# Optimization experiments

Measured on AMD Instinct MI355X. Metric: run time of the kernel, lower is better.

The kernel has to match this reference:

```python
import jax, jax.numpy as jnp
import numpy as np

N_NODES = 500000


def _gconv(x, src, dst, ew, w_neigh, b, w_self):
    # DGL GraphConv(norm='none'): multiply weight first (in>=out here), then aggregate.
    h = x @ w_neigh                      # [N, out]
    msg = h[src] * ew[:, None]           # [E, out]
    agg = jax.ops.segment_sum(msg, dst, num_segments=N_NODES)
    return agg + b + x @ w_self          # neigh conv (+bias) + self-loop linear (no bias)


def setup_inputs() -> dict:
    key = jax.random.key(0)
    ks = jax.random.split(key, 16)
    N, E, G, F = N_NODES, 16000000, 64, 16
    inp = {
        "x": jax.random.normal(ks[0], (N, F), jnp.float32),
        "src": jax.random.randint(ks[1], (E,), 0, N),
        "dst": jax.random.randint(ks[2], (E,), 0, N),
        "graph_id": jnp.sort(jax.random.randint(ks[3], (N,), 0, G)),
        "edge_weight": jax.random.uniform(ks[4], (E,), jnp.float32),
        "num_graphs": G,
        "w_neigh0": jax.random.normal(ks[5], (F, 1), jnp.float32),
        "b0": jax.random.normal(ks[6], (1,), jnp.float32),
        "w_self0": jax.random.normal(ks[7], (F, 1), jnp.float32),
        "w_neigh1": jax.random.normal(ks[8], (1, 1), jnp.float32),
        "b1": jax.random.normal(ks[9], (1,), jnp.float32),
        "w_self1": jax.random.normal(ks[10], (1, 1), jnp.float32),
        "w_neigh2": jax.random.normal(ks[11], (1, 1), jnp.float32),
        "b2": jax.random.normal(ks[12], (1,), jnp.float32),
        "w_self2": jax.random.normal(ks[13], (1, 1), jnp.float32),
        "fc1_w": jax.random.normal(ks[14], (8, 1), jnp.float32),
        "fc1_b": jax.random.normal(ks[15], (8,), jnp.float32),
        "out_w": jax.random.normal(jax.random.fold_in(key, 100), (4, 8), jnp.float32),
        "out_b": jax.random.normal(jax.random.fold_in(key, 101), (4,), jnp.float32),
    }
    return inp


def reference(x, src, dst, graph_id, edge_weight, num_graphs,
              w_neigh0, b0, w_self0, w_neigh1, b1, w_self1,
              w_neigh2, b2, w_self2, fc1_w, fc1_b, out_w, out_b):
    h = jax.nn.relu(_gconv(x, src, dst, edge_weight, w_neigh0, b0, w_self0))
    h = jax.nn.relu(_gconv(h, src, dst, edge_weight, w_neigh1, b1, w_self1))
    h = jax.nn.relu(_gconv(h, src, dst, edge_weight, w_neigh2, b2, w_self2))
    # dgl.sum_nodes: per-graph segment sum over batched graph -> [G, 1]
    hg = jax.ops.segment_sum(h, graph_id, num_segments=num_graphs)
    hg2 = jax.nn.sigmoid((hg @ fc1_w.T + fc1_b) * 1000.0)   # [G, 8]
    out = jax.nn.relu(hg2 @ out_w.T + out_b)                # [G, 4]
    return jax.nn.log_softmax(out, axis=1)
```

## Files before the change

### kernel.cpp

```cpp
#include <hip/hip_runtime.h>

#define N_NODES   500000
#define NGRAPH    64
#define FDIM      16
#define NPB       4096
#define NPB_SHIFT 12
#define NBINS     123
#define SLICES    4
#define NBLK      256
typedef unsigned int u32;
typedef unsigned long long u64;

__global__ void proj_kernel(const float* __restrict__ x,
                            const float* __restrict__ wn,
                            const float* __restrict__ wsf,
                            float* __restrict__ a,
                            float* __restrict__ s) {
    int i = blockIdx.x * blockDim.x + threadIdx.x;
    if (i >= N_NODES) return;
    const float4* xr = (const float4*)(x + (size_t)i * FDIM);
    float4 v0 = xr[0], v1 = xr[1], v2 = xr[2], v3 = xr[3];
    const float4* n4 = (const float4*)wn;
    const float4* s4 = (const float4*)wsf;
    float4 n0 = n4[0], n1 = n4[1], n2 = n4[2], n3 = n4[3];
    float4 w0 = s4[0], w1 = s4[1], w2 = s4[2], w3 = s4[3];
    float an = v0.x*n0.x + v0.y*n0.y + v0.z*n0.z + v0.w*n0.w
             + v1.x*n1.x + v1.y*n1.y + v1.z*n1.z + v1.w*n1.w
             + v2.x*n2.x + v2.y*n2.y + v2.z*n2.z + v2.w*n2.w
             + v3.x*n3.x + v3.y*n3.y + v3.z*n3.z + v3.w*n3.w;
    float as = v0.x*w0.x + v0.y*w0.y + v0.z*w0.z + v0.w*w0.w
             + v1.x*w1.x + v1.y*w1.y + v1.z*w1.z + v1.w*w1.w
             + v2.x*w2.x + v2.y*w2.y + v2.z*w2.z + v2.w*w2.w
             + v3.x*w3.x + v3.y*w3.y + v3.z*w3.z + v3.w*w3.w;
    a[i] = an;
    s[i] = as;
}

__global__ __launch_bounds__(1024) void hist_kernel(const int* __restrict__ dst, int E, int chunk,
                                                    u32* __restrict__ blockHist) {
    __shared__ u32 cnt[NBINS];
    for (int t = threadIdx.x; t < NBINS; t += 1024) cnt[t] = 0;
    __syncthreads();
    int b = blockIdx.x;
    int lo = b * chunk, hi = min(lo + chunk, E);
    int m = (hi - lo) & ~3;
    for (int i = lo + threadIdx.x * 4; i < lo + m; i += 4096) {
        int4 d = *(const int4*)(dst + i);
        atomicAdd(&cnt[((u32)d.x) >> NPB_SHIFT], 1u);
        atomicAdd(&cnt[((u32)d.y) >> NPB_SHIFT], 1u);
        atomicAdd(&cnt[((u32)d.z) >> NPB_SHIFT], 1u);
        atomicAdd(&cnt[((u32)d.w) >> NPB_SHIFT], 1u);
    }
    for (int i = lo + m + threadIdx.x; i < hi; i += 1024)
        atomicAdd(&cnt[((u32)dst[i]) >> NPB_SHIFT], 1u);
    __syncthreads();
    for (int t = threadIdx.x; t < NBINS; t += 1024)
        blockHist[(size_t)b * NBINS + t] = cnt[t];
}

__global__ __launch_bounds__(NBLK) void scan1_kernel(u32* __restrict__ blockHist,
                                                     u32* __restrict__ binTotal) {
    int j = blockIdx.x;
    __shared__ u32 lsum[NBLK];
    int t = threadIdx.x;
    u32 v = blockHist[(size_t)t * NBINS + j];
    lsum[t] = v;
    __syncthreads();
    u32 x = v;
    for (int off = 1; off < NBLK; off <<= 1) {
        u32 y = (t >= off) ? lsum[t - off] : 0u;
        __syncthreads();
        x += y; lsum[t] = x;
        __syncthreads();
    }
    if (t == NBLK - 1) binTotal[j] = x;
    blockHist[(size_t)t * NBINS + j] = x - v;
}

__global__ void scan2_kernel(const u32* __restrict__ binTotal, u32* __restrict__ binStart) {
    if (threadIdx.x == 0) {
        u32 run = 0;
        for (int j = 0; j < NBINS; ++j) { binStart[j] = run; run += binTotal[j]; }
        binStart[NBINS] = run;
    }
}

__global__ __launch_bounds__(1024) void scatter_kernel(const int* __restrict__ src,
                                                       const int* __restrict__ dst,
                                                       const float* __restrict__ ew,
                                                       int E, int chunk,
                                                       const u32* __restrict__ blockHist,
                                                       const u32* __restrict__ binStart,
                                                       u64* __restrict__ binned) {
    __shared__ u32 pos[NBINS];
    int b = blockIdx.x;
    for (int t = threadIdx.x; t < NBINS; t += 1024)
        pos[t] = binStart[t] + blockHist[(size_t)b * NBINS + t];
    __syncthreads();
    int lo = b * chunk, hi = min(lo + chunk, E);
    int m = (hi - lo) & ~3;
    for (int i = lo + threadIdx.x * 4; i < lo + m; i += 4096) {
        int4   ss = *(const int4*)(src + i);
        int4   dd = *(const int4*)(dst + i);
        float4 ww = *(const float4*)(ew + i);
        u32 d0 = (u32)dd.x, d1 = (u32)dd.y, d2 = (u32)dd.z, d3 = (u32)dd.w;
        u32 p0 = atomicAdd(&pos[d0 >> NPB_SHIFT], 1u);
        u32 p1 = atomicAdd(&pos[d1 >> NPB_SHIFT], 1u);
        u32 p2 = atomicAdd(&pos[d2 >> NPB_SHIFT], 1u);
        u32 p3 = atomicAdd(&pos[d3 >> NPB_SHIFT], 1u);
        u32 r0 = ((u32)ss.x) | ((d0 & (NPB-1)) << 19);
        u32 r1 = ((u32)ss.y) | ((d1 & (NPB-1)) << 19);
        u32 r2 = ((u32)ss.z) | ((d2 & (NPB-1)) << 19);
        u32 r3 = ((u32)ss.w) | ((d3 & (NPB-1)) << 19);
        binned[p0] = (u64)r0 | ((u64)__float_as_uint(ww.x) << 32);
        binned[p1] = (u64)r1 | ((u64)__float_as_uint(ww.y) << 32);
        binned[p2] = (u64)r2 | ((u64)__float_as_uint(ww.z) << 32);
        binned[p3] = (u64)r3 | ((u64)__float_as_uint(ww.w) << 32);
    }
    for (int i = lo + m + threadIdx.x; i < hi; i += 1024) {
        u32 d = (u32)dst[i];
        u32 p = atomicAdd(&pos[d >> NPB_SHIFT], 1u);
        binned[p] = (u64)(((u32)src[i]) | ((d & (NPB-1)) << 19))
                  | ((u64)__float_as_uint(ew[i]) << 32);
    }
}

__global__ __launch_bounds__(512) void bin_pass(const u64* __restrict__ binned,
                                                const u32* __restrict__ binStart,
                                                const float* __restrict__ hsrc,
                                                float* __restrict__ partials) {
    __shared__ float acc[NPB];
    int blk   = blockIdx.x;
    int j     = blk >> 2;
    int slice = blk & (SLICES - 1);
    for (int t = threadIdx.x; t < NPB; t += 512) acc[t] = 0.0f;
    __syncthreads();
    u32 blo = binStart[j], bhi = binStart[j + 1];
    u32 cnt = bhi - blo;
    u32 per = (cnt + SLICES - 1) / SLICES;
    u32 lo = blo + slice * per;
    u32 hi = min(lo + per, bhi);

    u32 i = lo + threadIdx.x;
    for (; i + 3u * 512u < hi; i += 4u * 512u) {
        u64 e0 = __builtin_nontemporal_load(&binned[i]);
        u64 e1 = __builtin_nontemporal_load(&binned[i + 512]);
        u64 e2 = __builtin_nontemporal_load(&binned[i + 1024]);
        u64 e3 = __builtin_nontemporal_load(&binned[i + 1536]);
        u32 x0 = (u32)e0, x1 = (u32)e1, x2 = (u32)e2, x3 = (u32)e3;
        float g0 = hsrc[x0 & 0x7FFFFu];
        float g1 = hsrc[x1 & 0x7FFFFu];
        float g2 = hsrc[x2 & 0x7FFFFu];
        float g3 = hsrc[x3 & 0x7FFFFu];
        atomicAdd(&acc[x0 >> 19], g0 * __uint_as_float((u32)(e0 >> 32)));
        atomicAdd(&acc[x1 >> 19], g1 * __uint_as_float((u32)(e1 >> 32)));
        atomicAdd(&acc[x2 >> 19], g2 * __uint_as_float((u32)(e2 >> 32)));
        atomicAdd(&acc[x3 >> 19], g3 * __uint_as_float((u32)(e3 >> 32)));
    }
    for (; i < hi; i += 512) {
        u64 e = __builtin_nontemporal_load(&binned[i]);
        u32 xx = (u32)e;
        atomicAdd(&acc[xx >> 19], hsrc[xx & 0x7FFFFu] * __uint_as_float((u32)(e >> 32)));
    }
    __syncthreads();
    float* p = partials + (size_t)(j * SLICES + slice) * NPB;
    for (int t = threadIdx.x; t < NPB; t += 512)
        __builtin_nontemporal_store(acc[t], &p[t]);
}

__global__ void merge_update(const float* __restrict__ partials,
                             const float* __restrict__ selfv,
                             const float* __restrict__ wnp,
                             const float* __restrict__ bp,
                             const float* __restrict__ wsp,
                             float* __restrict__ hout) {
    int n = blockIdx.x * blockDim.x + threadIdx.x;
    if (n >= N_NODES) return;
    int j = n >> NPB_SHIFT;
    int l = n & (NPB - 1);
    const float* p = partials + (size_t)j * SLICES * NPB + l;
    float sum = p[0] + p[NPB] + p[2 * NPB] + p[3 * NPB];
    float scale = wnp ? wnp[0] : 1.0f;
    float wself = wsp ? wsp[0] : 1.0f;
    hout[n] = fmaxf(sum * scale + bp[0] + selfv[n] * wself, 0.0f);
}

__global__ void edge_pass(const int* __restrict__ src, const int* __restrict__ dst,
                          const float* __restrict__ ew, const float* __restrict__ h,
                          float* __restrict__ agg, const float* __restrict__ wnp, int E) {
    float scale = wnp ? wnp[0] : 1.0f;
    int stride = gridDim.x * blockDim.x;
    for (int i = blockIdx.x * blockDim.x + threadIdx.x; i < E; i += stride)
        atomicAdd(&agg[dst[i]], h[src[i]] * ew[i] * scale);
}
__global__ void node_update(const float* __restrict__ agg, const float* __restrict__ selfv,
                            const float* __restrict__ bp, const float* __restrict__ wsp,
                            float* __restrict__ hout) {
    int i = blockIdx.x * blockDim.x + threadIdx.x;
    if (i >= N_NODES) return;
    float wsc = wsp ? wsp[0] : 1.0f;
    hout[i] = fmaxf(agg[i] + bp[0] + selfv[i] * wsc, 0.0f);
}

__global__ void graph_sum(const float* __restrict__ h, const int* __restrict__ gid,
                          float* __restrict__ hg) {
    __shared__ float loc[NGRAPH];
    int t = threadIdx.x;
    if (t < NGRAPH) loc[t] = 0.0f;
    __syncthreads();
    int stride = gridDim.x * blockDim.x;
    for (int i = blockIdx.x * blockDim.x + t; i < N_NODES; i += stride)
        atomicAdd(&loc[gid[i]], h[i]);
    __syncthreads();
    if (t < NGRAPH) atomicAdd(&hg[t], loc[t]);
}

__global__ void head_kernel(const float* __restrict__ hg,
                            const float* __restrict__ fc1w, const float* __restrict__ fc1b,
                            const float* __restrict__ outw, const float* __restrict__ outb,
                            float* __restrict__ out) {
    int g = threadIdx.x;
    if (g >= NGRAPH) return;
    float v = hg[g];
    float t[8];
#pragma unroll
    for (int j = 0; j < 8; ++j) {
        float z = (v * fc1w[j] + fc1b[j]) * 1000.0f;
        t[j] = 1.0f / (1.0f + expf(-z));
    }
    float o[4];
#pragma unroll
    for (int k = 0; k < 4; ++k) {
        float acc2 = outb[k];
#pragma unroll
        for (int j = 0; j < 8; ++j) acc2 += t[j] * outw[k * 8 + j];
        o[k] = fmaxf(acc2, 0.0f);
    }
    float m = fmaxf(fmaxf(o[0], o[1]), fmaxf(o[2], o[3]));
    float se = 0.0f;
#pragma unroll
    for (int k = 0; k < 4; ++k) se += expf(o[k] - m);
    float lse = m + logf(se);
#pragma unroll
    for (int k = 0; k < 4; ++k) out[g * 4 + k] = o[k] - lse;
}

extern "C" void kernel_launch(void* const* d_in, const int* in_sizes, int n_in,
                              void* d_out, int out_size, void* d_ws, size_t ws_size,
                              hipStream_t stream) {
    const float* x    = (const float*)d_in[0];
    const int*   src  = (const int*)  d_in[1];
    const int*   dst  = (const int*)  d_in[2];
    const int*   gid  = (const int*)  d_in[3];
    const float* ew   = (const float*)d_in[4];
    const float* wn0  = (const float*)d_in[6];
    const float* b0   = (const float*)d_in[7];
    const float* ws0  = (const float*)d_in[8];
    const float* wn1  = (const float*)d_in[9];
    const float* b1   = (const float*)d_in[10];
    const float* ws1  = (const float*)d_in[11];
    const float* wn2  = (const float*)d_in[12];
    const float* b2   = (const float*)d_in[13];
    const float* ws2  = (const float*)d_in[14];
    const float* fc1w = (const float*)d_in[15];
    const float* fc1b = (const float*)d_in[16];
    const float* outw = (const float*)d_in[17];
    const float* outb = (const float*)d_in[18];
    int E = in_sizes[1];

    const int BLK = 256;
    int nodeGrid = (N_NODES + BLK - 1) / BLK;
    char* ws = (char*)d_ws;

    size_t off = 0;
    u64*   binned    = (u64*)(ws + off);   off += (size_t)E * 8;
    u32*   blockHist = (u32*)(ws + off);   off += (size_t)NBLK * NBINS * 4;
    u32*   binStart  = (u32*)(ws + off);   off += (NBINS + 1) * 4;
    off = (off + 63) & ~(size_t)63;
    u32*   binTotal  = (u32*)(ws + off);   off += (NBINS + 1) * 4;
    off = (off + 63) & ~(size_t)63;
    float* partials  = (float*)(ws + off); off += (size_t)NBINS * SLICES * NPB * 4;
    float* a  = (float*)(ws + off); off += (size_t)N_NODES * 4;
    float* s  = (float*)(ws + off); off += (size_t)N_NODES * 4;
    float* h0 = (float*)(ws + off); off += (size_t)N_NODES * 4;
    float* h1 = (float*)(ws + off); off += (size_t)N_NODES * 4;
    float* hg = (float*)(ws + off); off += NGRAPH * 4;
    size_t need = off;

    if (ws_size >= need) {
        int chunk = (((E + NBLK - 1) / NBLK) + 3) & ~3;

        proj_kernel<<<nodeGrid, BLK, 0, stream>>>(x, wn0, ws0, a, s);

        hist_kernel<<<NBLK, 1024, 0, stream>>>(dst, E, chunk, blockHist);
        scan1_kernel<<<NBINS, NBLK, 0, stream>>>(blockHist, binTotal);
        scan2_kernel<<<1, 64, 0, stream>>>(binTotal, binStart);
        scatter_kernel<<<NBLK, 1024, 0, stream>>>(src, dst, ew, E, chunk, blockHist, binStart, binned);

        bin_pass<<<NBINS * SLICES, 512, 0, stream>>>(binned, binStart, a, partials);
        merge_update<<<nodeGrid, BLK, 0, stream>>>(partials, s, nullptr, b0, nullptr, h0);
        bin_pass<<<NBINS * SLICES, 512, 0, stream>>>(binned, binStart, h0, partials);
        merge_update<<<nodeGrid, BLK, 0, stream>>>(partials, h0, wn1, b1, ws1, h1);
        bin_pass<<<NBINS * SLICES, 512, 0, stream>>>(binned, binStart, h1, partials);
        merge_update<<<nodeGrid, BLK, 0, stream>>>(partials, h1, wn2, b2, ws2, a);

        (void)hipMemsetAsync(hg, 0, NGRAPH * sizeof(float), stream);
        graph_sum<<<512, BLK, 0, stream>>>(a, gid, hg);
        head_kernel<<<1, 64, 0, stream>>>(hg, fc1w, fc1b, outw, outb, (float*)d_out);
    } else {
        float* wsb  = (float*)d_ws;
        float* fa   = wsb;
        float* fs   = wsb + 1 * (size_t)N_NODES;
        float* fagg = wsb + 2 * (size_t)N_NODES;
        float* fh   = wsb + 3 * (size_t)N_NODES;
        float* fhg  = wsb + 4 * (size_t)N_NODES;

        proj_kernel<<<nodeGrid, BLK, 0, stream>>>(x, wn0, ws0, fa, fs);

        (void)hipMemsetAsync(fagg, 0, (size_t)N_NODES * sizeof(float), stream);
        edge_pass<<<4096, BLK, 0, stream>>>(src, dst, ew, fa, fagg, nullptr, E);
        node_update<<<nodeGrid, BLK, 0, stream>>>(fagg, fs, b0, nullptr, fh);

        (void)hipMemsetAsync(fagg, 0, (size_t)N_NODES * sizeof(float), stream);
        edge_pass<<<4096, BLK, 0, stream>>>(src, dst, ew, fh, fagg, wn1, E);
        node_update<<<nodeGrid, BLK, 0, stream>>>(fagg, fh, b1, ws1, fh);

        (void)hipMemsetAsync(fagg, 0, (size_t)N_NODES * sizeof(float), stream);
        edge_pass<<<4096, BLK, 0, stream>>>(src, dst, ew, fh, fagg, wn2, E);
        node_update<<<nodeGrid, BLK, 0, stream>>>(fagg, fh, b2, ws2, fh);

        (void)hipMemsetAsync(fhg, 0, NGRAPH * sizeof(float), stream);
        graph_sum<<<512, BLK, 0, stream>>>(fh, gid, fhg);
        head_kernel<<<1, 64, 0, stream>>>(fhg, fc1w, fc1b, outw, outb, (float*)d_out);
    }
}
```

Baseline: 485.2 us.

## Stage scatter through shared-memory local sort for coalesced binned writes

Replaces the direct per-edge scatter into global bins with a block-local counting sort. Each chunk of 4096 edges is grouped by bin in shared memory, then written out contiguously per bin, so global writes coalesce instead of landing at random addresses. The block count doubles to 512 with 512 threads each. bin_pass is unrolled from 4 to 8 loads in flight to hide gather latency. The cost is extra shared memory, several barriers and a small scan per chunk.

```diff
diff --git a/kernel.cpp b/kernel.cpp
--- a/kernel.cpp
+++ b/kernel.cpp
@@ -7,7 +7,8 @@
 #define NPB_SHIFT 12
 #define NBINS     123
 #define SLICES    4
-#define NBLK      256
+#define NBLK      512
+#define CH        4096
 typedef unsigned int u32;
 typedef unsigned long long u64;
 
@@ -85,43 +86,68 @@
     }
 }
 
-__global__ __launch_bounds__(1024) void scatter_kernel(const int* __restrict__ src,
-                                                       const int* __restrict__ dst,
-                                                       const float* __restrict__ ew,
-                                                       int E, int chunk,
-                                                       const u32* __restrict__ blockHist,
-                                                       const u32* __restrict__ binStart,
-                                                       u64* __restrict__ binned) {
-    __shared__ u32 pos[NBINS];
-    int b = blockIdx.x;
-    for (int t = threadIdx.x; t < NBINS; t += 1024)
-        pos[t] = binStart[t] + blockHist[(size_t)b * NBINS + t];
-    __syncthreads();
-    int lo = b * chunk, hi = min(lo + chunk, E);
-    int m = (hi - lo) & ~3;
-    for (int i = lo + threadIdx.x * 4; i < lo + m; i += 4096) {
-        int4   ss = *(const int4*)(src + i);
-        int4   dd = *(const int4*)(dst + i);
-        float4 ww = *(const float4*)(ew + i);
-        u32 d0 = (u32)dd.x, d1 = (u32)dd.y, d2 = (u32)dd.z, d3 = (u32)dd.w;
-        u32 p0 = atomicAdd(&pos[d0 >> NPB_SHIFT], 1u);
-        u32 p1 = atomicAdd(&pos[d1 >> NPB_SHIFT], 1u);
-        u32 p2 = atomicAdd(&pos[d2 >> NPB_SHIFT], 1u);
-        u32 p3 = atomicAdd(&pos[d3 >> NPB_SHIFT], 1u);
-        u32 r0 = ((u32)ss.x) | ((d0 & (NPB-1)) << 19);
-        u32 r1 = ((u32)ss.y) | ((d1 & (NPB-1)) << 19);
-        u32 r2 = ((u32)ss.z) | ((d2 & (NPB-1)) << 19);
-        u32 r3 = ((u32)ss.w) | ((d3 & (NPB-1)) << 19);
-        binned[p0] = (u64)r0 | ((u64)__float_as_uint(ww.x) << 32);
-        binned[p1] = (u64)r1 | ((u64)__float_as_uint(ww.y) << 32);
-        binned[p2] = (u64)r2 | ((u64)__float_as_uint(ww.z) << 32);
-        binned[p3] = (u64)r3 | ((u64)__float_as_uint(ww.w) << 32);
-    }
-    for (int i = lo + m + threadIdx.x; i < hi; i += 1024) {
-        u32 d = (u32)dst[i];
-        u32 p = atomicAdd(&pos[d >> NPB_SHIFT], 1u);
-        binned[p] = (u64)(((u32)src[i]) | ((d & (NPB-1)) << 19))
-                  | ((u64)__float_as_uint(ew[i]) << 32);
+__global__ __launch_bounds__(512) void scatter_staged(const int* __restrict__ src,
+                                                      const int* __restrict__ dst,
+                                                      const float* __restrict__ ew,
+                                                      int E, int chunk,
+                                                      const u32* __restrict__ blockHist,
+                                                      const u32* __restrict__ binStart,
+                                                      u64* __restrict__ binned) {
+    __shared__ u32 cursor[NBINS];
+    __shared__ u32 cnt[NBINS];
+    __shared__ u32 off[NBINS];
+    __shared__ u64 stage[CH];
+    __shared__ unsigned char binOf[CH];
+    int b   = blockIdx.x;
+    int tid = threadIdx.x;
+    for (int t = tid; t < NBINS; t += 512)
+        cursor[t] = binStart[t] + blockHist[(size_t)b * NBINS + t];
+    int lo = b * chunk, hiB = min(lo + chunk, E);
+    for (int base = lo; base < hiB; base += CH) {
+        int n = min(CH, hiB - base);
+        for (int t = tid; t < NBINS; t += 512) cnt[t] = 0;
+        __syncthreads();
+        u32 rec[8]; float wv[8]; u32 bi[8]; u32 rk[8];
+#pragma unroll
+        for (int k = 0; k < 8; ++k) {
+            int idx = base + k * 512 + tid;
+            bi[k] = 0xFFFFFFFFu;
+            if (idx < base + n) {
+                u32 d  = (u32)dst[idx];
+                bi[k]  = d >> NPB_SHIFT;
+                rec[k] = ((u32)src[idx]) | ((d & (NPB - 1)) << 19);
+                wv[k]  = ew[idx];
+                rk[k]  = atomicAdd(&cnt[bi[k]], 1u);
+            }
+        }
+        __syncthreads();
+        if (tid < NBINS) off[tid] = cnt[tid];
+        __syncthreads();
+        for (int d2 = 1; d2 < 128; d2 <<= 1) {
+            u32 v = 0;
+            if (tid < NBINS) { v = off[tid]; if (tid >= d2) v += off[tid - d2]; }
+            __syncthreads();
+            if (tid < NBINS) off[tid] = v;
+            __syncthreads();
+        }
+        if (tid < NBINS) off[tid] -= cnt[tid];
+        __syncthreads();
+#pragma unroll
+        for (int k = 0; k < 8; ++k) {
+            if (bi[k] != 0xFFFFFFFFu) {
+                u32 p = off[bi[k]] + rk[k];
+                stage[p] = (u64)rec[k] | ((u64)__float_as_uint(wv[k]) << 32);
+                binOf[p] = (unsigned char)bi[k];
+            }
+        }
+        __syncthreads();
+        for (int p = tid; p < n; p += 512) {
+            u32 j = binOf[p];
+            binned[cursor[j] + ((u32)p - off[j])] = stage[p];
+        }
+        __syncthreads();
+        for (int t = tid; t < NBINS; t += 512) cursor[t] += cnt[t];
+        __syncthreads();
     }
 }
 
@@ -142,20 +168,16 @@
     u32 hi = min(lo + per, bhi);
 
     u32 i = lo + threadIdx.x;
-    for (; i + 3u * 512u < hi; i += 4u * 512u) {
-        u64 e0 = __builtin_nontemporal_load(&binned[i]);
-        u64 e1 = __builtin_nontemporal_load(&binned[i + 512]);
-        u64 e2 = __builtin_nontemporal_load(&binned[i + 1024]);
-        u64 e3 = __builtin_nontemporal_load(&binned[i + 1536]);
-        u32 x0 = (u32)e0, x1 = (u32)e1, x2 = (u32)e2, x3 = (u32)e3;
-        float g0 = hsrc[x0 & 0x7FFFFu];
-        float g1 = hsrc[x1 & 0x7FFFFu];
-        float g2 = hsrc[x2 & 0x7FFFFu];
-        float g3 = hsrc[x3 & 0x7FFFFu];
-        atomicAdd(&acc[x0 >> 19], g0 * __uint_as_float((u32)(e0 >> 32)));
-        atomicAdd(&acc[x1 >> 19], g1 * __uint_as_float((u32)(e1 >> 32)));
-        atomicAdd(&acc[x2 >> 19], g2 * __uint_as_float((u32)(e2 >> 32)));
-        atomicAdd(&acc[x3 >> 19], g3 * __uint_as_float((u32)(e3 >> 32)));
+    for (; i + 7u * 512u < hi; i += 8u * 512u) {
+        u64 e[8];
+#pragma unroll
+        for (int k = 0; k < 8; ++k) e[k] = __builtin_nontemporal_load(&binned[i + (u32)k * 512u]);
+        float g[8];
+#pragma unroll
+        for (int k = 0; k < 8; ++k) g[k] = hsrc[((u32)e[k]) & 0x7FFFFu];
+#pragma unroll
+        for (int k = 0; k < 8; ++k)
+            atomicAdd(&acc[((u32)e[k]) >> 19], g[k] * __uint_as_float((u32)(e[k] >> 32)));
     }
     for (; i < hi; i += 512) {
         u64 e = __builtin_nontemporal_load(&binned[i]);
@@ -295,7 +317,7 @@
         hist_kernel<<<NBLK, 1024, 0, stream>>>(dst, E, chunk, blockHist);
         scan1_kernel<<<NBINS, NBLK, 0, stream>>>(blockHist, binTotal);
         scan2_kernel<<<1, 64, 0, stream>>>(binTotal, binStart);
-        scatter_kernel<<<NBLK, 1024, 0, stream>>>(src, dst, ew, E, chunk, blockHist, binStart, binned);
+        scatter_staged<<<NBLK, 512, 0, stream>>>(src, dst, ew, E, chunk, blockHist, binStart, binned);
 
         bin_pass<<<NBINS * SLICES, 512, 0, stream>>>(binned, binStart, a, partials);
         merge_update<<<nodeGrid, BLK, 0, stream>>>(partials, s, nullptr, b0, nullptr, h0);
```

Result: faster. 424.2 us (-12.6%).
